# Kernel optimization log

Measured on AMD Instinct MI355X. Metric: run time of the kernel, lower is better.

## Reference

```python
import jax, jax.numpy as jnp
import numpy as np


def setup_inputs() -> dict:
    key = jax.random.key(0)
    k1, k2, k3 = jax.random.split(key, 3)
    bs, r, d = 4, 4096, 64
    G = jax.random.uniform(k1, (bs, d), dtype=jnp.float32)          # eigenvalues (non-negative)
    V = jax.random.normal(k2, (bs, r, d), dtype=jnp.float32)        # eigenvectors / spectral embedding
    weights = jax.random.uniform(k3, (1,), dtype=jnp.float32)       # learned scalar t
    return {"G": G, "V": V, "weights": weights}


def reference(G, V, weights):
    # Original: eVs = diag(max(G,0)^(2t)); y = E@eVs@Phi2^T + Phi2@eVs@E^T - 2*Phi@eVs@Phi^T
    # Since eVs is diagonal, this is the weighted pairwise squared distance:
    # y[b,i,j] = sum_k w[b,k] * (V[b,i,k] - V[b,j,k])^2 with w = max(G,0)^(2t).
    t = weights[0]
    w = jnp.maximum(G, jnp.zeros_like(G)) ** (2.0 * t)   # (bs, d)
    Vw = V * w[:, None, :]                               # (bs, r, d) elementwise diag scaling
    s = jnp.sum(Vw * V, axis=-1)                         # (bs, r): weighted squared norms
    cross = jnp.einsum('brd,bsd->brs', Vw, V)            # (bs, r, r)
    y = s[:, :, None] + s[:, None, :] - 2.0 * cross
    return y
```

## Files before the change

### kernel.cpp

```cpp
#include <hip/hip_runtime.h>
#include <hip/hip_bf16.h>


typedef __attribute__((ext_vector_type(8))) short bf16x8;
typedef __attribute__((ext_vector_type(4))) float f32x4;

constexpr int BS = 4, R = 4096, D = 64;
constexpr int LS = 260;

__device__ __forceinline__ void barrier_lds_only() {
    asm volatile("s_waitcnt lgkmcnt(0)" ::: "memory");
    __builtin_amdgcn_sched_barrier(0);
    __builtin_amdgcn_s_barrier();
    __builtin_amdgcn_sched_barrier(0);
}

__global__ __launch_bounds__(256) void prep_kernel(
    const float* __restrict__ G, const float* __restrict__ V,
    const float* __restrict__ wt,
    __hip_bfloat16* __restrict__ u_bf, float* __restrict__ s)
{
    int row  = blockIdx.x * 4 + (threadIdx.x >> 6);
    int lane = threadIdx.x & 63;
    if (row >= BS * R) return;
    int b = row / R;

    float t  = wt[0];
    float g  = fmaxf(G[b * D + lane], 0.0f);
    float sw = powf(g, t);
    float u  = sw * V[(size_t)row * D + lane];

    __hip_bfloat16 ub = __float2bfloat16(u);
    u_bf[(size_t)row * D + lane] = ub;

    float uf   = __bfloat162float(ub);
    float prod = uf * uf;
    #pragma unroll
    for (int off = 32; off; off >>= 1) prod += __shfl_down(prod, off);
    if (lane == 0) s[row] = prod;
}

__global__ __launch_bounds__(512) void dist_kernel(
    const short* __restrict__ U, const float* __restrict__ s,
    float* __restrict__ out)
{
    __shared__ float lds[64 * LS];

    int lane = threadIdx.x & 63;
    int wave = threadIdx.x >> 6;
    int wr   = wave >> 2;
    int wc   = wave & 3;

    int b  = blockIdx.z;
    int jb = blockIdx.x * 256;
    int i0 = blockIdx.y * 128;

    const short* Ap = U + ((size_t)b * R + i0 + wr * 64) * D;
    const short* Bp = U + ((size_t)b * R + jb + wc * 64) * D;
    const float* sb = s + (size_t)b * R;

    int lrow = lane & 15;
    int kgrp = lane >> 4;

    bf16x8 a[4][2];
    #pragma unroll
    for (int rb = 0; rb < 4; ++rb)
        #pragma unroll
        for (int ks = 0; ks < 2; ++ks)
            a[rb][ks] = *(const bf16x8*)(Ap + (rb * 16 + lrow) * D + ks * 32 + kgrp * 8);

    f32x4 acc[4][4];
    #pragma unroll
    for (int rb = 0; rb < 4; ++rb)
        #pragma unroll
        for (int jt = 0; jt < 4; ++jt)
            acc[rb][jt] = f32x4{0.f, 0.f, 0.f, 0.f};

    #pragma unroll
    for (int jt = 0; jt < 4; ++jt) {
        const short* Bt = Bp + jt * 16 * D;
        bf16x8 b0 = *(const bf16x8*)(Bt + lrow * D +      kgrp * 8);
        bf16x8 b1 = *(const bf16x8*)(Bt + lrow * D + 32 + kgrp * 8);
        #pragma unroll
        for (int rb = 0; rb < 4; ++rb) {
            acc[rb][jt] = __builtin_amdgcn_mfma_f32_16x16x32_bf16(a[rb][0], b0, acc[rb][jt], 0, 0, 0);
            acc[rb][jt] = __builtin_amdgcn_mfma_f32_16x16x32_bf16(a[rb][1], b1, acc[rb][jt], 0, 0, 0);
        }
    }

    float si_lane = sb[i0 + wr * 64 + lane];

    float* outb = out + ((size_t)b * R + i0) * R + jb;

    #pragma unroll
    for (int c = 0; c < 2; ++c) {
        if (wr == c) {
            #pragma unroll
            for (int rb = 0; rb < 4; ++rb) {
                #pragma unroll
                for (int rg = 0; rg < 4; ++rg) {
                    int rl = rb * 16 + kgrp * 4 + rg;
                    float si = __shfl(si_lane, rl);
                    #pragma unroll
                    for (int jt = 0; jt < 4; ++jt) {
                        float sj = sb[jb + wc * 64 + jt * 16 + lrow];
                        float y  = si + sj - 2.0f * acc[rb][jt][rg];
                        lds[rl * LS + wc * 64 + jt * 16 + lrow] = y;
                    }
                }
            }
        }
        barrier_lds_only();

        #pragma unroll
        for (int r = 0; r < 8; ++r) {
            int rl = wave * 8 + r;
            f32x4 v = *(const f32x4*)&lds[rl * LS + lane * 4];
            __builtin_nontemporal_store(v,
                (f32x4*)(outb + (size_t)(c * 64 + rl) * R + lane * 4));
        }
        if (c == 0) barrier_lds_only();
    }
}

extern "C" void kernel_launch(void* const* d_in, const int* in_sizes, int n_in,
                              void* d_out, int out_size, void* d_ws, size_t ws_size,
                              hipStream_t stream) {
    const float* G  = (const float*)d_in[0];
    const float* V  = (const float*)d_in[1];
    const float* wt = (const float*)d_in[2];
    float* out = (float*)d_out;

    char* ws = (char*)d_ws;
    __hip_bfloat16* u_bf = (__hip_bfloat16*)ws;
    float*          s    = (float*)        (ws + (size_t)BS * R * D * 2);

    prep_kernel<<<BS * R / 4, 256, 0, stream>>>(G, V, wt, u_bf, s);

    dim3 grid(R / 256, R / 128, BS);
    dist_kernel<<<grid, 512, 0, stream>>>((const short*)u_bf, s, out);
}
```

Baseline: 64.66 us.

## Make distance kernel persistent with prefetch of next tile's fragments

Replaces the 2048-block grid with 256 persistent blocks that each loop over 8 output tiles. While the current tile's epilogue runs, the bf16 fragments for the next tile are loaded into registers, and their MFMAs are issued after the stores. This removes per-block launch and ramp-up cost and overlaps global loads with the output-store phase. The cost is higher register pressure from the extra B fragments, and an extra barrier per chunk.

```diff
diff --git a/kernel.cpp b/kernel.cpp
--- a/kernel.cpp
+++ b/kernel.cpp
@@ -7,6 +7,11 @@
 
 constexpr int BS = 4, R = 4096, D = 64;
 constexpr int LS = 260;
+constexpr int TILES_X = 16;
+constexpr int TILES_Y = 32;
+constexpr int NTILES  = TILES_X * TILES_Y * BS;
+constexpr int NBLK    = 256;
+constexpr int KITER   = NTILES / NBLK;
 
 __device__ __forceinline__ void barrier_lds_only() {
     asm volatile("s_waitcnt lgkmcnt(0)" ::: "memory");
@@ -50,76 +55,93 @@
     int wave = threadIdx.x >> 6;
     int wr   = wave >> 2;
     int wc   = wave & 3;
-
-    int b  = blockIdx.z;
-    int jb = blockIdx.x * 256;
-    int i0 = blockIdx.y * 128;
-
-    const short* Ap = U + ((size_t)b * R + i0 + wr * 64) * D;
-    const short* Bp = U + ((size_t)b * R + jb + wc * 64) * D;
-    const float* sb = s + (size_t)b * R;
-
     int lrow = lane & 15;
     int kgrp = lane >> 4;
+    int bid  = blockIdx.x;
 
     bf16x8 a[4][2];
-    #pragma unroll
-    for (int rb = 0; rb < 4; ++rb)
+    bf16x8 bf[4][2];
+    f32x4  acc[4][4];
+
+    auto load_frags = [&](int tid) {
+        int x = tid & (TILES_X - 1);
+        int y = (tid >> 4) & (TILES_Y - 1);
+        int z = tid >> 9;
+        const short* Ap = U + ((size_t)z * R + y * 128 + wr * 64) * D;
+        const short* Bp = U + ((size_t)z * R + x * 256 + wc * 64) * D;
         #pragma unroll
-        for (int ks = 0; ks < 2; ++ks)
-            a[rb][ks] = *(const bf16x8*)(Ap + (rb * 16 + lrow) * D + ks * 32 + kgrp * 8);
-
-    f32x4 acc[4][4];
-    #pragma unroll
-    for (int rb = 0; rb < 4; ++rb)
+        for (int rb = 0; rb < 4; ++rb)
+            #pragma unroll
+            for (int ks = 0; ks < 2; ++ks)
+                a[rb][ks] = *(const bf16x8*)(Ap + (rb * 16 + lrow) * D + ks * 32 + kgrp * 8);
         #pragma unroll
         for (int jt = 0; jt < 4; ++jt)
-            acc[rb][jt] = f32x4{0.f, 0.f, 0.f, 0.f};
+            #pragma unroll
+            for (int ks = 0; ks < 2; ++ks)
+                bf[jt][ks] = *(const bf16x8*)(Bp + (jt * 16 + lrow) * D + ks * 32 + kgrp * 8);
+    };
 
-    #pragma unroll
-    for (int jt = 0; jt < 4; ++jt) {
-        const short* Bt = Bp + jt * 16 * D;
-        bf16x8 b0 = *(const bf16x8*)(Bt + lrow * D +      kgrp * 8);
-        bf16x8 b1 = *(const bf16x8*)(Bt + lrow * D + 32 + kgrp * 8);
+    auto mfma_all = [&]() {
         #pragma unroll
-        for (int rb = 0; rb < 4; ++rb) {
-            acc[rb][jt] = __builtin_amdgcn_mfma_f32_16x16x32_bf16(a[rb][0], b0, acc[rb][jt], 0, 0, 0);
-            acc[rb][jt] = __builtin_amdgcn_mfma_f32_16x16x32_bf16(a[rb][1], b1, acc[rb][jt], 0, 0, 0);
-        }
-    }
-
-    float si_lane = sb[i0 + wr * 64 + lane];
-
-    float* outb = out + ((size_t)b * R + i0) * R + jb;
-
-    #pragma unroll
-    for (int c = 0; c < 2; ++c) {
-        if (wr == c) {
+        for (int rb = 0; rb < 4; ++rb)
+            #pragma unroll
+            for (int jt = 0; jt < 4; ++jt)
+                acc[rb][jt] = f32x4{0.f, 0.f, 0.f, 0.f};
+        #pragma unroll
+        for (int jt = 0; jt < 4; ++jt)
             #pragma unroll
             for (int rb = 0; rb < 4; ++rb) {
+                acc[rb][jt] = __builtin_amdgcn_mfma_f32_16x16x32_bf16(a[rb][0], bf[jt][0], acc[rb][jt], 0, 0, 0);
+                acc[rb][jt] = __builtin_amdgcn_mfma_f32_16x16x32_bf16(a[rb][1], bf[jt][1], acc[rb][jt], 0, 0, 0);
+            }
+    };
+
+    load_frags(bid);
+    mfma_all();
+
+    for (int k = 0; k < KITER; ++k) {
+        int tid = bid + k * NBLK;
+        int x = tid & (TILES_X - 1);
+        int y = (tid >> 4) & (TILES_Y - 1);
+        int z = tid >> 9;
+
+        if (k + 1 < KITER) load_frags(bid + (k + 1) * NBLK);
+
+        const float* sb = s + (size_t)z * R;
+        float si_lane = sb[y * 128 + wr * 64 + lane];
+        float* outb = out + ((size_t)z * R + y * 128) * R + x * 256;
+
+        #pragma unroll
+        for (int c = 0; c < 2; ++c) {
+            if (wr == c) {
                 #pragma unroll
-                for (int rg = 0; rg < 4; ++rg) {
-                    int rl = rb * 16 + kgrp * 4 + rg;
-                    float si = __shfl(si_lane, rl);
+                for (int rb = 0; rb < 4; ++rb) {
                     #pragma unroll
-                    for (int jt = 0; jt < 4; ++jt) {
-                        float sj = sb[jb + wc * 64 + jt * 16 + lrow];
-                        float y  = si + sj - 2.0f * acc[rb][jt][rg];
-                        lds[rl * LS + wc * 64 + jt * 16 + lrow] = y;
+                    for (int rg = 0; rg < 4; ++rg) {
+                        int rl = rb * 16 + kgrp * 4 + rg;
+                        float si = __shfl(si_lane, rl);
+                        #pragma unroll
+                        for (int jt = 0; jt < 4; ++jt) {
+                            float sj = sb[x * 256 + wc * 64 + jt * 16 + lrow];
+                            float y_ = si + sj - 2.0f * acc[rb][jt][rg];
+                            lds[rl * LS + wc * 64 + jt * 16 + lrow] = y_;
+                        }
                     }
                 }
             }
+            barrier_lds_only();
+
+            #pragma unroll
+            for (int r = 0; r < 8; ++r) {
+                int rl = wave * 8 + r;
+                f32x4 v = *(const f32x4*)&lds[rl * LS + lane * 4];
+                __builtin_nontemporal_store(v,
+                    (f32x4*)(outb + (size_t)(c * 64 + rl) * R + lane * 4));
+            }
+            barrier_lds_only();
         }
-        barrier_lds_only();
 
-        #pragma unroll
-        for (int r = 0; r < 8; ++r) {
-            int rl = wave * 8 + r;
-            f32x4 v = *(const f32x4*)&lds[rl * LS + lane * 4];
-            __builtin_nontemporal_store(v,
-                (f32x4*)(outb + (size_t)(c * 64 + rl) * R + lane * 4));
-        }
-        if (c == 0) barrier_lds_only();
+        if (k + 1 < KITER) mfma_all();
     }
 }
 
@@ -137,6 +159,5 @@
 
     prep_kernel<<<BS * R / 4, 256, 0, stream>>>(G, V, wt, u_bf, s);
 
-    dim3 grid(R / 256, R / 128, BS);
-    dist_kernel<<<grid, 512, 0, stream>>>((const short*)u_bf, s, out);
+    dist_kernel<<<NBLK, 512, 0, stream>>>((const short*)u_bf, s, out);
 }
```

New measurement: 70.77 us. +9.5%, slower.

## Retile distance kernel to 16-row by 1024-column blocks per workgroup

Applied to the files above, without the earlier changes.

Changes the output tile from 128x256 to 16x1024. Each wave now computes a 16x128 strip using one shared A fragment, and the sj and si loads are hoisted into registers. The LDS staging buffer shrinks to 8 rows by 1024 columns, and each wave writes 4 KB row segments. The aim is to make the output stores long and contiguous and to cut LDS and register use. The cost is loading more B data per output element, which is likely minor since the kernel is bound by writing the 256 MB output.

```diff
diff --git a/kernel.cpp b/kernel.cpp
--- a/kernel.cpp
+++ b/kernel.cpp
@@ -6,7 +6,8 @@
 typedef __attribute__((ext_vector_type(4))) float f32x4;
 
 constexpr int BS = 4, R = 4096, D = 64;
-constexpr int LS = 260;
+constexpr int BN  = 1024;
+constexpr int LSW = BN + 4;
 
 __device__ __forceinline__ void barrier_lds_only() {
     asm volatile("s_waitcnt lgkmcnt(0)" ::: "memory");
@@ -44,80 +45,68 @@
     const short* __restrict__ U, const float* __restrict__ s,
     float* __restrict__ out)
 {
-    __shared__ float lds[64 * LS];
+    __shared__ float lds[8 * LSW];
 
     int lane = threadIdx.x & 63;
     int wave = threadIdx.x >> 6;
-    int wr   = wave >> 2;
-    int wc   = wave & 3;
-
-    int b  = blockIdx.z;
-    int jb = blockIdx.x * 256;
-    int i0 = blockIdx.y * 128;
-
-    const short* Ap = U + ((size_t)b * R + i0 + wr * 64) * D;
-    const short* Bp = U + ((size_t)b * R + jb + wc * 64) * D;
-    const float* sb = s + (size_t)b * R;
-
     int lrow = lane & 15;
     int kgrp = lane >> 4;
 
-    bf16x8 a[4][2];
+    int b  = blockIdx.z;
+    int jb = blockIdx.x * BN;
+    int i0 = blockIdx.y * 16;
+    int jw = wave * 128;
+
+    const short* Ap = U + ((size_t)b * R + i0) * D;
+    const short* Bp = U + ((size_t)b * R + jb + jw) * D;
+    const float* sb = s + (size_t)b * R;
+
+    bf16x8 a0 = *(const bf16x8*)(Ap + lrow * D +      kgrp * 8);
+    bf16x8 a1 = *(const bf16x8*)(Ap + lrow * D + 32 + kgrp * 8);
+
+    f32x4 acc[8];
     #pragma unroll
-    for (int rb = 0; rb < 4; ++rb)
-        #pragma unroll
-        for (int ks = 0; ks < 2; ++ks)
-            a[rb][ks] = *(const bf16x8*)(Ap + (rb * 16 + lrow) * D + ks * 32 + kgrp * 8);
-
-    f32x4 acc[4][4];
-    #pragma unroll
-    for (int rb = 0; rb < 4; ++rb)
-        #pragma unroll
-        for (int jt = 0; jt < 4; ++jt)
-            acc[rb][jt] = f32x4{0.f, 0.f, 0.f, 0.f};
+    for (int jt = 0; jt < 8; ++jt) acc[jt] = f32x4{0.f, 0.f, 0.f, 0.f};
 
     #pragma unroll
-    for (int jt = 0; jt < 4; ++jt) {
+    for (int jt = 0; jt < 8; ++jt) {
         const short* Bt = Bp + jt * 16 * D;
         bf16x8 b0 = *(const bf16x8*)(Bt + lrow * D +      kgrp * 8);
         bf16x8 b1 = *(const bf16x8*)(Bt + lrow * D + 32 + kgrp * 8);
-        #pragma unroll
-        for (int rb = 0; rb < 4; ++rb) {
-            acc[rb][jt] = __builtin_amdgcn_mfma_f32_16x16x32_bf16(a[rb][0], b0, acc[rb][jt], 0, 0, 0);
-            acc[rb][jt] = __builtin_amdgcn_mfma_f32_16x16x32_bf16(a[rb][1], b1, acc[rb][jt], 0, 0, 0);
-        }
+        acc[jt] = __builtin_amdgcn_mfma_f32_16x16x32_bf16(a0, b0, acc[jt], 0, 0, 0);
+        acc[jt] = __builtin_amdgcn_mfma_f32_16x16x32_bf16(a1, b1, acc[jt], 0, 0, 0);
     }
 
-    float si_lane = sb[i0 + wr * 64 + lane];
+    float si_lane = sb[i0 + (lane & 15)];
+    float si[4];
+    #pragma unroll
+    for (int rg = 0; rg < 4; ++rg) si[rg] = __shfl(si_lane, kgrp * 4 + rg);
+    float sj[8];
+    #pragma unroll
+    for (int jt = 0; jt < 8; ++jt) sj[jt] = sb[jb + jw + jt * 16 + lrow];
 
     float* outb = out + ((size_t)b * R + i0) * R + jb;
 
     #pragma unroll
     for (int c = 0; c < 2; ++c) {
-        if (wr == c) {
+        if ((kgrp >> 1) == c) {
+            int lr4 = (kgrp & 1) * 4;
             #pragma unroll
-            for (int rb = 0; rb < 4; ++rb) {
+            for (int rg = 0; rg < 4; ++rg) {
                 #pragma unroll
-                for (int rg = 0; rg < 4; ++rg) {
-                    int rl = rb * 16 + kgrp * 4 + rg;
-                    float si = __shfl(si_lane, rl);
-                    #pragma unroll
-                    for (int jt = 0; jt < 4; ++jt) {
-                        float sj = sb[jb + wc * 64 + jt * 16 + lrow];
-                        float y  = si + sj - 2.0f * acc[rb][jt][rg];
-                        lds[rl * LS + wc * 64 + jt * 16 + lrow] = y;
-                    }
+                for (int jt = 0; jt < 8; ++jt) {
+                    float y = si[rg] + sj[jt] - 2.0f * acc[jt][rg];
+                    lds[(lr4 + rg) * LSW + jw + jt * 16 + lrow] = y;
                 }
             }
         }
         barrier_lds_only();
 
         #pragma unroll
-        for (int r = 0; r < 8; ++r) {
-            int rl = wave * 8 + r;
-            f32x4 v = *(const f32x4*)&lds[rl * LS + lane * 4];
+        for (int t = 0; t < 4; ++t) {
+            f32x4 v = *(const f32x4*)&lds[wave * LSW + t * 256 + lane * 4];
             __builtin_nontemporal_store(v,
-                (f32x4*)(outb + (size_t)(c * 64 + rl) * R + lane * 4));
+                (f32x4*)(outb + (size_t)(c * 8 + wave) * R + t * 256 + lane * 4));
         }
         if (c == 0) barrier_lds_only();
     }
@@ -137,6 +126,6 @@
 
     prep_kernel<<<BS * R / 4, 256, 0, stream>>>(G, V, wt, u_bf, s);
 
-    dim3 grid(R / 256, R / 128, BS);
+    dim3 grid(R / BN, R / 16, BS);
     dist_kernel<<<grid, 512, 0, stream>>>((const short*)u_bf, s, out);
 }
```

Measured after the change: 90.95 us. 1.41x slower.
